# Kernel tuning notes

Hardware: AMD Instinct MI355X
Metric: run time of the kernel (lower is better)

The kernel has to match this reference:

```python
import jax, jax.numpy as jnp
import numpy as np

N_NODES = 100000
N_EDGES = 600000
N_FEAT = 128


def setup_inputs() -> dict:
    key = jax.random.key(0)
    k1, k2, k3 = jax.random.split(key, 3)
    x = jax.random.normal(k1, (N_NODES, N_FEAT), dtype=jnp.float32)
    W = jax.random.normal(k2, (N_FEAT, N_FEAT), dtype=jnp.float32) / np.sqrt(N_FEAT)
    b = jnp.zeros((N_FEAT,), dtype=jnp.float32)
    edge_index = jax.random.randint(k3, (2, N_EDGES), 0, N_NODES, dtype=jnp.int64)
    return {"x": x, "W": W, "b": b, "edge_index": edge_index}


def reference(x, W, b, edge_index):
    # GCNConv: out = D^{-1/2} (A + I) D^{-1/2} (x @ W) + b, then ReLU
    n = x.shape[0]
    loop = jnp.arange(n, dtype=edge_index.dtype)
    src = jnp.concatenate([edge_index[0], loop])  # [E + N]
    dst = jnp.concatenate([edge_index[1], loop])  # [E + N]

    # degree of target nodes (includes self-loops)
    ones = jnp.ones(src.shape[0], dtype=x.dtype)
    deg = jax.ops.segment_sum(ones, dst, num_segments=n)  # [N]
    dinv = jnp.where(deg > 0, jax.lax.rsqrt(deg), 0.0)
    norm = dinv[src] * dinv[dst]  # [E + N]

    h = x @ W  # [N, F]
    msg = h[src] * norm[:, None]  # gather + scale, [E + N, F]
    agg = jax.ops.segment_sum(msg, dst, num_segments=n)  # scatter-add, [N, F]
    return jax.nn.relu(agg + b)
```

## Files before the change

### kernel.cpp

```cpp
#include <hip/hip_runtime.h>

#define NN 100000
#define NE 600000
#define F  128
#define CAP 48

#define NBLK   ((NN + 255) / 256)
#define GEMM_B ((NN + 127) / 128)
#define FILL_B ((NE + 255) / 256)

#define OFF_DEG  0
#define OFF_FLAG (960*1024)
#define OFF_WT   (1024*1024)
#define OFF_G    (2048*1024)
#define OFF_CSR  (28672*1024)

typedef __attribute__((ext_vector_type(8))) short bf16x8;
typedef __attribute__((ext_vector_type(16))) float f32x16;

__device__ inline unsigned short f2b(float f) {
    unsigned int u = __builtin_bit_cast(unsigned int, f);
    u += 0x7fffu + ((u >> 16) & 1u);
    return (unsigned short)(u >> 16);
}
__device__ inline float b_lo(unsigned int v) {
    return __builtin_bit_cast(float, v << 16);
}
__device__ inline float b_hi(unsigned int v) {
    return __builtin_bit_cast(float, v & 0xffff0000u);
}

__global__ __launch_bounds__(256) void k_init(const int* __restrict__ ei,
                                              const float* __restrict__ W,
                                              int* __restrict__ deg,
                                              int* __restrict__ flag,
                                              unsigned short* __restrict__ wtg) {
    int i = blockIdx.x * 256 + threadIdx.x;
    if (i < NN) deg[i] = 0;
    if (i < F * F) {
        int k = i >> 7, n = i & 127;
        wtg[n * F + k] = f2b(W[k * F + n]);
    }
    if (blockIdx.x == 0) {
        __shared__ int cnt;
        if (threadIdx.x == 0) cnt = 0;
        __syncthreads();
        if (ei[2 * threadIdx.x + 1] == 0) atomicAdd(&cnt, 1);
        __syncthreads();
        if (threadIdx.x == 0) *flag = (cnt > 128) ? 1 : 0;
    }
}

__global__ __launch_bounds__(256) void k_gemm_fill(const float* __restrict__ x,
                                                   const unsigned short* __restrict__ wtg,
                                                   unsigned short* __restrict__ gb,
                                                   const int* __restrict__ ei,
                                                   const int* __restrict__ flag,
                                                   int* __restrict__ deg,
                                                   int* __restrict__ csr) {
    if (blockIdx.x >= GEMM_B) {
        int e = (blockIdx.x - GEMM_B) * 256 + threadIdx.x;
        if (e < NE) {
            int f = *flag;
            int src = ei[e << f];
            int dst = ei[(NE + e) << f];
            int slot = atomicAdd(&deg[dst], 1);
            if (slot < CAP) csr[dst * CAP + slot] = src;
        }
        return;
    }

    const int tid  = threadIdx.x;
    const int w    = tid >> 6;
    const int lane = tid & 63;
    const int m    = lane & 31;
    const int half = lane >> 5;
    const int row0 = blockIdx.x * 128;

    const int arow = min(row0 + 32 * w + m, NN - 1);
    const float*          xr = x   + (long)arow * F + half * 8;
    const unsigned short* wr = wtg + m * F + half * 8;

    f32x16 acc[4];
#pragma unroll
    for (int t = 0; t < 4; ++t)
#pragma unroll
        for (int j = 0; j < 16; ++j) acc[t][j] = 0.f;

#pragma unroll
    for (int kc = 0; kc < 8; ++kc) {
        float4 a0 = *(const float4*)(xr + kc * 16);
        float4 a1 = *(const float4*)(xr + kc * 16 + 4);
        bf16x8 a;
        a[0] = (short)f2b(a0.x); a[1] = (short)f2b(a0.y);
        a[2] = (short)f2b(a0.z); a[3] = (short)f2b(a0.w);
        a[4] = (short)f2b(a1.x); a[5] = (short)f2b(a1.y);
        a[6] = (short)f2b(a1.z); a[7] = (short)f2b(a1.w);
#pragma unroll
        for (int nt = 0; nt < 4; ++nt) {
            bf16x8 bfr = *(const bf16x8*)(wr + nt * 32 * F + kc * 16);
            acc[nt] = __builtin_amdgcn_mfma_f32_32x32x16_bf16(a, bfr, acc[nt], 0, 0, 0);
        }
    }

    const int rbase = 32 * w + 4 * half;
#pragma unroll
    for (int nt = 0; nt < 4; ++nt) {
#pragma unroll
        for (int reg = 0; reg < 16; ++reg) {
            int grow = row0 + rbase + (reg & 3) + 8 * (reg >> 2);
            if (grow < NN)
                gb[(long)grow * F + nt * 32 + m] = f2b(acc[nt][reg]);
        }
    }
}

__global__ __launch_bounds__(256) void k_gather(const int* __restrict__ deg,
                                                const int* __restrict__ csr,
                                                const unsigned short* __restrict__ gb,
                                                const float* __restrict__ b,
                                                float* __restrict__ out) {
    int n = blockIdx.x * 4 + (threadIdx.x >> 6);
    if (n >= NN) return;
    const int lane = threadIdx.x & 63;
    const int l16  = lane & 15;
    const int grp  = lane >> 4;
    const int dn   = deg[n];
    const float dvn = rsqrtf((float)(dn + 1));
    const long base = (long)n * CAP;

    float a[8];
    if (grp == 0) {
        uint4 v = *(const uint4*)(gb + (long)n * F + l16 * 8);
        a[0] = b_lo(v.x) * dvn; a[1] = b_hi(v.x) * dvn;
        a[2] = b_lo(v.y) * dvn; a[3] = b_hi(v.y) * dvn;
        a[4] = b_lo(v.z) * dvn; a[5] = b_hi(v.z) * dvn;
        a[6] = b_lo(v.w) * dvn; a[7] = b_hi(v.w) * dvn;
    } else {
#pragma unroll
        for (int j = 0; j < 8; ++j) a[j] = 0.f;
    }

    int p = grp;
    for (; p + 4 < dn; p += 8) {
        int s0 = csr[base + p];
        int s1 = csr[base + p + 4];
        float d0 = rsqrtf((float)(deg[s0] + 1));
        float d1 = rsqrtf((float)(deg[s1] + 1));
        uint4 v0 = *(const uint4*)(gb + (long)s0 * F + l16 * 8);
        uint4 v1 = *(const uint4*)(gb + (long)s1 * F + l16 * 8);
        a[0] += b_lo(v0.x) * d0; a[1] += b_hi(v0.x) * d0;
        a[2] += b_lo(v0.y) * d0; a[3] += b_hi(v0.y) * d0;
        a[4] += b_lo(v0.z) * d0; a[5] += b_hi(v0.z) * d0;
        a[6] += b_lo(v0.w) * d0; a[7] += b_hi(v0.w) * d0;
        a[0] += b_lo(v1.x) * d1; a[1] += b_hi(v1.x) * d1;
        a[2] += b_lo(v1.y) * d1; a[3] += b_hi(v1.y) * d1;
        a[4] += b_lo(v1.z) * d1; a[5] += b_hi(v1.z) * d1;
        a[6] += b_lo(v1.w) * d1; a[7] += b_hi(v1.w) * d1;
    }
    if (p < dn) {
        int s0 = csr[base + p];
        float d0 = rsqrtf((float)(deg[s0] + 1));
        uint4 v0 = *(const uint4*)(gb + (long)s0 * F + l16 * 8);
        a[0] += b_lo(v0.x) * d0; a[1] += b_hi(v0.x) * d0;
        a[2] += b_lo(v0.y) * d0; a[3] += b_hi(v0.y) * d0;
        a[4] += b_lo(v0.z) * d0; a[5] += b_hi(v0.z) * d0;
        a[6] += b_lo(v0.w) * d0; a[7] += b_hi(v0.w) * d0;
    }

#pragma unroll
    for (int j = 0; j < 8; ++j) {
        a[j] += __shfl_xor(a[j], 16);
        a[j] += __shfl_xor(a[j], 32);
    }

    if (grp == 0) {
        float4 b0 = *(const float4*)(b + l16 * 8);
        float4 b1 = *(const float4*)(b + l16 * 8 + 4);
        float4 o0, o1;
        o0.x = fmaxf(a[0] * dvn + b0.x, 0.f);
        o0.y = fmaxf(a[1] * dvn + b0.y, 0.f);
        o0.z = fmaxf(a[2] * dvn + b0.z, 0.f);
        o0.w = fmaxf(a[3] * dvn + b0.w, 0.f);
        o1.x = fmaxf(a[4] * dvn + b1.x, 0.f);
        o1.y = fmaxf(a[5] * dvn + b1.y, 0.f);
        o1.z = fmaxf(a[6] * dvn + b1.z, 0.f);
        o1.w = fmaxf(a[7] * dvn + b1.w, 0.f);
        long obase = (long)n * F + l16 * 8;
        *(float4*)(out + obase)     = o0;
        *(float4*)(out + obase + 4) = o1;
    }
}

extern "C" void kernel_launch(void* const* d_in, const int* in_sizes, int n_in,
                              void* d_out, int out_size, void* d_ws, size_t ws_size,
                              hipStream_t stream) {
    const float* x  = (const float*)d_in[0];
    const float* W  = (const float*)d_in[1];
    const float* b  = (const float*)d_in[2];
    const int*   ei = (const int*)d_in[3];
    float* out = (float*)d_out;

    char* ws = (char*)d_ws;
    int*            deg  = (int*)(ws + OFF_DEG);
    int*            flag = (int*)(ws + OFF_FLAG);
    unsigned short* wtg  = (unsigned short*)(ws + OFF_WT);
    unsigned short* gb   = (unsigned short*)(ws + OFF_G);
    int*            csr  = (int*)(ws + OFF_CSR);

    k_init<<<NBLK, 256, 0, stream>>>(ei, W, deg, flag, wtg);
    k_gemm_fill<<<GEMM_B + FILL_B, 256, 0, stream>>>(x, wtg, gb, ei, flag, deg, csr);
    k_gather<<<(NN + 3) / 4, 256, 0, stream>>>(deg, csr, gb, b, out);
}
```

Before: 211.9 us.

## Stage x tile in swizzled LDS as bf16 and pre-pack W in MFMA fragment order

```diff
diff --git a/kernel.cpp b/kernel.cpp
--- a/kernel.cpp
+++ b/kernel.cpp
@@ -34,12 +34,16 @@
                                               const float* __restrict__ W,
                                               int* __restrict__ deg,
                                               int* __restrict__ flag,
-                                              unsigned short* __restrict__ wtg) {
+                                              unsigned short* __restrict__ pb) {
     int i = blockIdx.x * 256 + threadIdx.x;
     if (i < NN) deg[i] = 0;
     if (i < F * F) {
-        int k = i >> 7, n = i & 127;
-        wtg[n * F + k] = f2b(W[k * F + n]);
+        int j  = i & 7;
+        int l  = (i >> 3) & 63;
+        int tt = i >> 9;
+        int k  = (tt >> 2) * 16 + ((l >> 5) << 3) + j;
+        int n  = (tt & 3) * 32 + (l & 31);
+        pb[i] = f2b(W[k * F + n]);
     }
     if (blockIdx.x == 0) {
         __shared__ int cnt;
@@ -52,7 +56,7 @@
 }
 
 __global__ __launch_bounds__(256) void k_gemm_fill(const float* __restrict__ x,
-                                                   const unsigned short* __restrict__ wtg,
+                                                   const unsigned short* __restrict__ pb,
                                                    unsigned short* __restrict__ gb,
                                                    const int* __restrict__ ei,
                                                    const int* __restrict__ flag,
@@ -70,35 +74,44 @@
         return;
     }
 
-    const int tid  = threadIdx.x;
-    const int w    = tid >> 6;
-    const int lane = tid & 63;
+    __shared__ unsigned short xs[128 * 128];
+    const int t    = threadIdx.x;
+    const int row0 = blockIdx.x * 128;
+
+#pragma unroll 4
+    for (int it = 0; it < 16; ++it) {
+        int r  = it * 8 + (t >> 5);
+        int gr = min(row0 + r, NN - 1);
+        float4 v = *(const float4*)(x + (long)gr * F + (t & 31) * 4);
+        unsigned int lo = (unsigned int)f2b(v.x) | ((unsigned int)f2b(v.y) << 16);
+        unsigned int hi = (unsigned int)f2b(v.z) | ((unsigned int)f2b(v.w) << 16);
+        int bcol = ((t & 31) * 8) ^ ((r & 15) << 4);
+        uint2 u; u.x = lo; u.y = hi;
+        *(uint2*)((char*)xs + r * 256 + bcol) = u;
+    }
+    __syncthreads();
+
+    const int w    = t >> 6;
+    const int lane = t & 63;
     const int m    = lane & 31;
     const int half = lane >> 5;
-    const int row0 = blockIdx.x * 128;
-
-    const int arow = min(row0 + 32 * w + m, NN - 1);
-    const float*          xr = x   + (long)arow * F + half * 8;
-    const unsigned short* wr = wtg + m * F + half * 8;
 
     f32x16 acc[4];
 #pragma unroll
-    for (int t = 0; t < 4; ++t)
-#pragma unroll
-        for (int j = 0; j < 16; ++j) acc[t][j] = 0.f;
+    for (int nt = 0; nt < 4; ++nt)
+#pragma unroll
+        for (int j = 0; j < 16; ++j) acc[nt][j] = 0.f;
+
+    const int r = 32 * w + m;
+    const unsigned short* pw = pb + lane * 8;
 
 #pragma unroll
     for (int kc = 0; kc < 8; ++kc) {
-        float4 a0 = *(const float4*)(xr + kc * 16);
-        float4 a1 = *(const float4*)(xr + kc * 16 + 4);
-        bf16x8 a;
-        a[0] = (short)f2b(a0.x); a[1] = (short)f2b(a0.y);
-        a[2] = (short)f2b(a0.z); a[3] = (short)f2b(a0.w);
-        a[4] = (short)f2b(a1.x); a[5] = (short)f2b(a1.y);
-        a[6] = (short)f2b(a1.z); a[7] = (short)f2b(a1.w);
+        int bcol = (kc * 32 + half * 16) ^ ((r & 15) << 4);
+        bf16x8 a = *(const bf16x8*)((const char*)xs + r * 256 + bcol);
 #pragma unroll
         for (int nt = 0; nt < 4; ++nt) {
-            bf16x8 bfr = *(const bf16x8*)(wr + nt * 32 * F + kc * 16);
+            bf16x8 bfr = *(const bf16x8*)(pw + (kc * 4 + nt) * 512);
             acc[nt] = __builtin_amdgcn_mfma_f32_32x32x16_bf16(a, bfr, acc[nt], 0, 0, 0);
         }
     }
@@ -204,11 +217,11 @@
     char* ws = (char*)d_ws;
     int*            deg  = (int*)(ws + OFF_DEG);
     int*            flag = (int*)(ws + OFF_FLAG);
-    unsigned short* wtg  = (unsigned short*)(ws + OFF_WT);
+    unsigned short* pb   = (unsigned short*)(ws + OFF_WT);
     unsigned short* gb   = (unsigned short*)(ws + OFF_G);
     int*            csr  = (int*)(ws + OFF_CSR);
 
-    k_init<<<NBLK, 256, 0, stream>>>(ei, W, deg, flag, wtg);
-    k_gemm_fill<<<GEMM_B + FILL_B, 256, 0, stream>>>(x, wtg, gb, ei, flag, deg, csr);
+    k_init<<<NBLK, 256, 0, stream>>>(ei, W, deg, flag, pb);
+    k_gemm_fill<<<GEMM_B + FILL_B, 256, 0, stream>>>(x, pb, gb, ei, flag, deg, csr);
     k_gather<<<(NN + 3) / 4, 256, 0, stream>>>(deg, csr, gb, b, out);
 }
```

Measured after the change: 198.8 us. -6.2%, faster.
